# Performance work log

Hardware: AMD Instinct MI355X
Metric: run time of the kernel (lower is better)

## Reference

```python
import jax, jax.numpy as jnp
import numpy as np

NP, P, NS = 5, 5, 15  # body parts, joints per part, segments per scale


def _gauss_forward(x):
    # x: (batch, nb_frames, joints=NP*P, coordinates, 1)
    b, T, J, C, _ = x.shape
    inp = x.reshape(b, T, NP, P, C, 1)
    # lengths of the 6 temporal windows: full, two halves, three thirds
    seg_lens = [T, T // 2, T - T // 2, T // 3, T // 3, T - 2 * (T // 3)]
    outs = []
    for L in seg_lens:
        nb_fr = L // NS
        # first NS-1 segments of nb_fr frames each, always starting at frame 0
        head = inp[:, :(NS - 1) * nb_fr].reshape(b, NS - 1, nb_fr, NP, P, C, 1)
        mu_h = head.mean(axis=2)                    # (b, NS-1, NP, P, C, 1)
        xc = head - mu_h[:, :, None]
        cov_h = jnp.einsum('bkfnpci,bkfnpdi->bknpcd', xc, xc) / nb_fr
        # last segment runs to the END of the full sequence (faithful to original)
        tail = inp[:, (NS - 1) * nb_fr:]
        rest = tail.shape[1]
        mu_t = tail.mean(axis=1)                    # (b, NP, P, C, 1)
        xt = tail - mu_t[:, None]
        cov_t = jnp.einsum('bfnpci,bfnpdi->bnpcd', xt, xt) / rest
        mu = jnp.concatenate([mu_h, mu_t[:, None]], axis=1)    # (b, NS, NP, P, C, 1)
        cov = jnp.concatenate([cov_h, cov_t[:, None]], axis=1)  # (b, NS, NP, P, C, C)
        # match torch layout (b, NP, NS, P, ...)
        mu = jnp.transpose(mu, (0, 2, 1, 3, 4, 5))
        cov = jnp.transpose(cov, (0, 2, 1, 3, 4, 5))
        muT = jnp.swapaxes(mu, -1, -2)
        elt00 = cov + mu @ muT                       # E[xx^T]
        ones = jnp.ones(mu.shape[:-2] + (1, 1), dtype=x.dtype)
        top = jnp.concatenate([elt00, mu], axis=-1)
        bot = jnp.concatenate([muT, ones], axis=-1)
        outs.append(jnp.concatenate([top, bot], axis=-2))
    # (b, 6, NP, NS, P, C+1, C+1)
    return jnp.stack(outs, axis=1)


def setup_inputs() -> dict:
    key = jax.random.key(0)
    x = jax.random.normal(key, (256, 2048, 25, 3, 1), dtype=jnp.float32)
    return {"x": x}


def reference(x):
    return _gauss_forward(x)
```

## Files before the change

kernel.cpp:

```cpp
#include <hip/hip_runtime.h>
#include <hip/hip_bf16.h>
#include <stdint.h>


#define NPIECE_MAX 64
#define IDXPK 0x9210287517640543ull

struct Tab {
    int n;
    uint32_t p[NPIECE_MAX];
    uint32_t meta[NPIECE_MAX];
};

__global__ __launch_bounds__(1024) void fused_kernel(const float* __restrict__ x,
                                                     float* __restrict__ out, Tab tab) {
    __shared__ float sx[2][3760];
    __shared__ float red[6 * 225 + 16];
    int tid = threadIdx.x;
    int b   = blockIdx.x;
    const float* xb = x + (size_t)b * 153600;
    int wv = tid >> 6, ln = tid & 63;

    for (int i = tid; i < 6 * 225 + 16; i += 1024) red[i] = 0.f;

    {
        uint32_t pk = tab.p[0];
        int f0 = pk & 0xffff, L = (int)(pk >> 16);
        int w0 = f0 * 75, base_f = w0 & ~3;
        int nv4 = (w0 - base_f + L * 75 + 3) >> 2;
        const float4* src = (const float4*)(xb + base_f);
        int i = wv * 64 + ln;
        if (i < nv4)
            __builtin_amdgcn_global_load_lds(
                (const __attribute__((address_space(1))) void*)(src + i),
                (__attribute__((address_space(3))) void*)(&sx[0][wv * 256]), 16, 0, 0);
    }

    int cell = tid >> 2, q = tid & 3;
    int j  = cell / 9, si = cell - j * 9;
    int k3 = si - 3;
    int ia = (si < 3) ? si : (k3 < 3 ? 0 : (k3 < 5 ? 1 : 2));
    int ib = (si < 3) ? si : (k3 < 3 ? k3 : (k3 < 5 ? k3 - 2 : 2));
    bool single = (si < 3);
    int off0 = q * 75 + j * 3;

    __syncthreads();

    int n = tab.n;
    for (int p = 0; p < n; ++p) {
        uint32_t pk = tab.p[p];
        int f0 = pk & 0xffff, L = (int)(pk >> 16);
        int shift = (f0 * 75) & 3;
        int buf = p & 1;

        if (p + 1 < n) {
            uint32_t pk2 = tab.p[p + 1];
            int g0 = pk2 & 0xffff, L2 = (int)(pk2 >> 16);
            int w0 = g0 * 75, base_f = w0 & ~3;
            int nv4 = (w0 - base_f + L2 * 75 + 3) >> 2;
            const float4* src = (const float4*)(xb + base_f);
            int i = wv * 64 + ln;
            if (i < nv4)
                __builtin_amdgcn_global_load_lds(
                    (const __attribute__((address_space(1))) void*)(src + i),
                    (__attribute__((address_space(3))) void*)(&sx[buf ^ 1][wv * 256]), 16, 0, 0);
        }

        uint32_t mt = tab.meta[p];
        if (tid < 900) {
            const float* s = &sx[buf][shift];
            float acc = 0.f;
            int off = off0;
            for (int t = q; t < L; t += 4, off += 300) {
                float a  = s[off + ia];
                float bb = s[off + ib];
                acc += single ? a : a * bb;
            }
            acc += __shfl_xor(acc, 1);
            acc += __shfl_xor(acc, 2);
            if (q == 0) {
                int c0 = mt & 15, c1 = (mt >> 4) & 15, c2 = (mt >> 8) & 15;
                red[((c0 & 1)) * 225 + cell]     += acc;
                red[(2 + (c1 & 1)) * 225 + cell] += acc;
                red[(4 + (c2 & 1)) * 225 + cell] += acc;
            }
        }

        uint32_t em = (mt >> 12) & 7;
        if (em) {
            __syncthreads();
            float4* ob4 = (float4*)(out + (size_t)b * 36000);
            for (int st = 0; st < 3; ++st) {
                if (!((em >> st) & 1)) continue;
                int ch  = (mt >> (4 * st)) & 15;
                int ns  = (st == 0) ? 136 : (st == 1) ? 68 : 45;
                int nfr = (ch == 14) ? (2048 - 14 * ns) : ns;
                float inv = 1.0f / (float)nfr;
                int slot = st * 2 + (ch & 1);
                int ndup = st + 1;
                int so0  = (st == 0) ? 0 : (st == 1) ? 1 : 3;
                int tot  = ndup * 100;
                for (int i2 = tid; i2 < tot; i2 += 1024) {
                    int dup = i2 / 100;
                    int r2  = i2 - dup * 100;
                    int jj  = r2 >> 2, r = r2 & 3;
                    int np_ = jj / 5, pp = jj - np_ * 5;
                    const float* rb = &red[slot * 225 + jj * 9];
                    uint64_t pkk = IDXPK >> (16 * r);
                    float4 v;
                    v.x = rb[(int)(pkk & 15)] * inv;
                    v.y = rb[(int)((pkk >> 4) & 15)] * inv;
                    v.z = rb[(int)((pkk >> 8) & 15)] * inv;
                    v.w = (r == 3) ? 1.0f : rb[(int)((pkk >> 12) & 15)] * inv;
                    ob4[(so0 + dup) * 1500 + np_ * 300 + ch * 20 + pp * 4 + r] = v;
                }
            }
            __syncthreads();
            if (tid < 225) {
                for (int st = 0; st < 3; ++st) {
                    if (!((em >> st) & 1)) continue;
                    int ch = (mt >> (4 * st)) & 15;
                    red[(st * 2 + (ch & 1)) * 225 + tid] = 0.f;
                }
            }
        }
        __syncthreads();
    }
}

static void build_tab(Tab& tab) {
    unsigned char isb[2049];
    for (int i = 0; i <= 2048; ++i) isb[i] = 0;
    isb[2048] = 1;
    for (int k = 1; k <= 14; ++k) { isb[45 * k] = 1; isb[68 * k] = 1; isb[136 * k] = 1; }
    int n = 0, prev = 0;
    for (int f = 1; f <= 2048; ++f) {
        if (!isb[f]) continue;
        int len = f - prev;
        int npc = (len + 49) / 50;
        int base = len / npc, rem = len % npc;
        int s = prev;
        for (int i = 0; i < npc && n < NPIECE_MAX; ++i) {
            int l = base + (i < rem ? 1 : 0);
            tab.p[n++] = (uint32_t)(s | (l << 16));
            s += l;
        }
        prev = f;
    }
    tab.n = n;
    const int nst[3] = {136, 68, 45};
    for (int i = 0; i < n; ++i) {
        int f0 = tab.p[i] & 0xffff;
        int f1 = f0 + (int)(tab.p[i] >> 16);
        uint32_t m = 0;
        for (int st = 0; st < 3; ++st) {
            int ns = nst[st];
            int c = f0 / ns; if (c > 14) c = 14;
            int bnd = (c == 14) ? 2048 : (c + 1) * ns;
            m |= (uint32_t)c << (4 * st);
            if (f1 == bnd) m |= 1u << (12 + st);
        }
        tab.meta[i] = m;
    }
}

extern "C" void kernel_launch(void* const* d_in, const int* in_sizes, int n_in,
                              void* d_out, int out_size, void* d_ws, size_t ws_size,
                              hipStream_t stream) {
    const float* x = (const float*)d_in[0];
    float* out = (float*)d_out;
    Tab tab;
    build_tab(tab);
    fused_kernel<<<256, 1024, 0, stream>>>(x, out, tab);
}
```

Measured before the change: 251.0 us.

## Accumulate per-joint moments in registers with prefix marks, larger segments

Replaces the per-cell LDS accumulation (900 threads, 4 lanes per covariance entry) with 200 threads that each read a joint's three coordinates and accumulate all nine moments in registers. The running sums are differenced against per-scale marks at segment boundaries, so only the boundary pieces are reduced through shuffles. Pieces now span whole boundary-to-boundary intervals, with larger LDS buffers loaded in three chunks, which cuts the number of iterations and barriers. Output writes move to a single wave, and the barriers become raw s_waitcnt plus s_barrier. In exchange, only about 200 of 1024 threads do the compute, so per-thread serial work grows and parallelism drops.

```diff
diff --git a/kernel.cpp b/kernel.cpp
--- a/kernel.cpp
+++ b/kernel.cpp
@@ -1,111 +1,123 @@
 #include <hip/hip_runtime.h>
-#include <hip/hip_bf16.h>
 #include <stdint.h>
 
 
-#define NPIECE_MAX 64
+#define NSEG_MAX 40
 #define IDXPK 0x9210287517640543ull
 
 struct Tab {
     int n;
-    uint32_t p[NPIECE_MAX];
-    uint32_t meta[NPIECE_MAX];
+    uint32_t p[NSEG_MAX];
+    uint32_t meta[NSEG_MAX];
 };
 
-__global__ __launch_bounds__(1024) void fused_kernel(const float* __restrict__ x,
-                                                     float* __restrict__ out, Tab tab) {
-    __shared__ float sx[2][3760];
-    __shared__ float red[6 * 225 + 16];
+__device__ __forceinline__ void ebar() {
+    asm volatile("s_waitcnt lgkmcnt(0)\n\ts_barrier" ::: "memory");
+}
+
+__global__ __launch_bounds__(1024) void fused2(const float* __restrict__ x,
+                                               float* __restrict__ out, Tab tab) {
+    __shared__ float sx[2][10816];
+    __shared__ float red[240];
     int tid = threadIdx.x;
-    int b   = blockIdx.x;
+    int b = blockIdx.x;
     const float* xb = x + (size_t)b * 153600;
-    int wv = tid >> 6, ln = tid & 63;
+    int wv = tid >> 6;
 
-    for (int i = tid; i < 6 * 225 + 16; i += 1024) red[i] = 0.f;
+    float run[9], mark0[9], mark1[9], mark2[9];
+    #pragma unroll
+    for (int i = 0; i < 9; ++i) { run[i]=0.f; mark0[i]=0.f; mark1[i]=0.f; mark2[i]=0.f; }
+
+    int j = tid >> 3, ph = tid & 7;
 
     {
         uint32_t pk = tab.p[0];
         int f0 = pk & 0xffff, L = (int)(pk >> 16);
-        int w0 = f0 * 75, base_f = w0 & ~3;
-        int nv4 = (w0 - base_f + L * 75 + 3) >> 2;
-        const float4* src = (const float4*)(xb + base_f);
-        int i = wv * 64 + ln;
-        if (i < nv4)
-            __builtin_amdgcn_global_load_lds(
-                (const __attribute__((address_space(1))) void*)(src + i),
-                (__attribute__((address_space(3))) void*)(&sx[0][wv * 256]), 16, 0, 0);
+        int w0 = f0 * 75, bf = w0 & ~3;
+        int nv4 = (w0 - bf + L * 75 + 3) >> 2;
+        const float4* src = (const float4*)(xb + bf);
+        #pragma unroll
+        for (int k = 0; k < 3; ++k) {
+            int i = k * 1024 + tid;
+            if (i < nv4)
+                __builtin_amdgcn_global_load_lds(
+                    (const __attribute__((address_space(1))) void*)(src + i),
+                    (__attribute__((address_space(3))) void*)(&sx[0][(k * 1024 + wv * 64) * 4]),
+                    16, 0, 0);
+        }
     }
-
-    int cell = tid >> 2, q = tid & 3;
-    int j  = cell / 9, si = cell - j * 9;
-    int k3 = si - 3;
-    int ia = (si < 3) ? si : (k3 < 3 ? 0 : (k3 < 5 ? 1 : 2));
-    int ib = (si < 3) ? si : (k3 < 3 ? k3 : (k3 < 5 ? k3 - 2 : 2));
-    bool single = (si < 3);
-    int off0 = q * 75 + j * 3;
-
-    __syncthreads();
 
     int n = tab.n;
     for (int p = 0; p < n; ++p) {
+        __syncthreads();
+        int buf = p & 1;
+        if (p + 1 < n) {
+            uint32_t pk = tab.p[p + 1];
+            int f0 = pk & 0xffff, L = (int)(pk >> 16);
+            int w0 = f0 * 75, bf = w0 & ~3;
+            int nv4 = (w0 - bf + L * 75 + 3) >> 2;
+            const float4* src = (const float4*)(xb + bf);
+            #pragma unroll
+            for (int k = 0; k < 3; ++k) {
+                int i = k * 1024 + tid;
+                if (i < nv4)
+                    __builtin_amdgcn_global_load_lds(
+                        (const __attribute__((address_space(1))) void*)(src + i),
+                        (__attribute__((address_space(3))) void*)(&sx[buf ^ 1][(k * 1024 + wv * 64) * 4]),
+                        16, 0, 0);
+            }
+        }
+
         uint32_t pk = tab.p[p];
         int f0 = pk & 0xffff, L = (int)(pk >> 16);
-        int shift = (f0 * 75) & 3;
-        int buf = p & 1;
-
-        if (p + 1 < n) {
-            uint32_t pk2 = tab.p[p + 1];
-            int g0 = pk2 & 0xffff, L2 = (int)(pk2 >> 16);
-            int w0 = g0 * 75, base_f = w0 & ~3;
-            int nv4 = (w0 - base_f + L2 * 75 + 3) >> 2;
-            const float4* src = (const float4*)(xb + base_f);
-            int i = wv * 64 + ln;
-            if (i < nv4)
-                __builtin_amdgcn_global_load_lds(
-                    (const __attribute__((address_space(1))) void*)(src + i),
-                    (__attribute__((address_space(3))) void*)(&sx[buf ^ 1][wv * 256]), 16, 0, 0);
+        if (tid < 200) {
+            const float* s = &sx[buf][(f0 * 75) & 3];
+            int l0 = (ph - f0) & 7;
+            for (int l = l0; l < L; l += 8) {
+                const float* q = s + l * 75 + j * 3;
+                float a = q[0], bb = q[1], c = q[2];
+                run[0] += a;      run[1] += bb;     run[2] += c;
+                run[3] += a * a;  run[4] += a * bb; run[5] += a * c;
+                run[6] += bb * bb; run[7] += bb * c; run[8] += c * c;
+            }
         }
 
         uint32_t mt = tab.meta[p];
-        if (tid < 900) {
-            const float* s = &sx[buf][shift];
-            float acc = 0.f;
-            int off = off0;
-            for (int t = q; t < L; t += 4, off += 300) {
-                float a  = s[off + ia];
-                float bb = s[off + ib];
-                acc += single ? a : a * bb;
+        uint32_t em = mt >> 12;
+        for (int st = 0; st < 3; ++st) {
+            if (!((em >> st) & 1)) continue;
+            int ch = (mt >> (4 * st)) & 15;
+            if (tid < 200) {
+                float* mk = (st == 0) ? mark0 : (st == 1) ? mark1 : mark2;
+                float d[9];
+                #pragma unroll
+                for (int i = 0; i < 9; ++i) { d[i] = run[i] - mk[i]; mk[i] = run[i]; }
+                #pragma unroll
+                for (int i = 0; i < 9; ++i) {
+                    d[i] += __shfl_xor(d[i], 1);
+                    d[i] += __shfl_xor(d[i], 2);
+                    d[i] += __shfl_xor(d[i], 4);
+                }
+                float v = d[0];
+                #pragma unroll
+                for (int i = 1; i < 8; ++i) v = (ph == i) ? d[i] : v;
+                red[j * 9 + ph] = v;
+                if (ph == 0) red[j * 9 + 8] = d[8];
             }
-            acc += __shfl_xor(acc, 1);
-            acc += __shfl_xor(acc, 2);
-            if (q == 0) {
-                int c0 = mt & 15, c1 = (mt >> 4) & 15, c2 = (mt >> 8) & 15;
-                red[((c0 & 1)) * 225 + cell]     += acc;
-                red[(2 + (c1 & 1)) * 225 + cell] += acc;
-                red[(4 + (c2 & 1)) * 225 + cell] += acc;
-            }
-        }
-
-        uint32_t em = (mt >> 12) & 7;
-        if (em) {
-            __syncthreads();
-            float4* ob4 = (float4*)(out + (size_t)b * 36000);
-            for (int st = 0; st < 3; ++st) {
-                if (!((em >> st) & 1)) continue;
-                int ch  = (mt >> (4 * st)) & 15;
+            ebar();
+            if (wv == 15) {
                 int ns  = (st == 0) ? 136 : (st == 1) ? 68 : 45;
                 int nfr = (ch == 14) ? (2048 - 14 * ns) : ns;
                 float inv = 1.0f / (float)nfr;
-                int slot = st * 2 + (ch & 1);
-                int ndup = st + 1;
-                int so0  = (st == 0) ? 0 : (st == 1) ? 1 : 3;
-                int tot  = ndup * 100;
-                for (int i2 = tid; i2 < tot; i2 += 1024) {
-                    int dup = i2 / 100;
-                    int r2  = i2 - dup * 100;
-                    int jj  = r2 >> 2, r = r2 & 3;
+                int so0 = (st == 0) ? 0 : (st == 1) ? 1 : 3;
+                int Q = (st + 1) * 100;
+                float4* ob4 = (float4*)(out + (size_t)b * 36000);
+                int lane = tid - 960;
+                for (int q2 = lane; q2 < Q; q2 += 64) {
+                    int dup = q2 / 100, r2 = q2 - dup * 100;
+                    int jj = r2 >> 2, r = r2 & 3;
                     int np_ = jj / 5, pp = jj - np_ * 5;
-                    const float* rb = &red[slot * 225 + jj * 9];
+                    const float* rb = &red[jj * 9];
                     uint64_t pkk = IDXPK >> (16 * r);
                     float4 v;
                     v.x = rb[(int)(pkk & 15)] * inv;
@@ -115,16 +127,8 @@
                     ob4[(so0 + dup) * 1500 + np_ * 300 + ch * 20 + pp * 4 + r] = v;
                 }
             }
-            __syncthreads();
-            if (tid < 225) {
-                for (int st = 0; st < 3; ++st) {
-                    if (!((em >> st) & 1)) continue;
-                    int ch = (mt >> (4 * st)) & 15;
-                    red[(st * 2 + (ch & 1)) * 225 + tid] = 0.f;
-                }
-            }
+            ebar();
         }
-        __syncthreads();
     }
 }
 
@@ -133,35 +137,23 @@
     for (int i = 0; i <= 2048; ++i) isb[i] = 0;
     isb[2048] = 1;
     for (int k = 1; k <= 14; ++k) { isb[45 * k] = 1; isb[68 * k] = 1; isb[136 * k] = 1; }
+    const int nst[3] = {136, 68, 45};
     int n = 0, prev = 0;
     for (int f = 1; f <= 2048; ++f) {
         if (!isb[f]) continue;
-        int len = f - prev;
-        int npc = (len + 49) / 50;
-        int base = len / npc, rem = len % npc;
-        int s = prev;
-        for (int i = 0; i < npc && n < NPIECE_MAX; ++i) {
-            int l = base + (i < rem ? 1 : 0);
-            tab.p[n++] = (uint32_t)(s | (l << 16));
-            s += l;
+        tab.p[n] = (uint32_t)(prev | ((f - prev) << 16));
+        uint32_t m = 0;
+        for (int st = 0; st < 3; ++st) {
+            int ns = nst[st];
+            int c = prev / ns; if (c > 14) c = 14;
+            int bnd = (c == 14) ? 2048 : (c + 1) * ns;
+            m |= (uint32_t)c << (4 * st);
+            if (f == bnd) m |= 1u << (12 + st);
         }
+        tab.meta[n++] = m;
         prev = f;
     }
     tab.n = n;
-    const int nst[3] = {136, 68, 45};
-    for (int i = 0; i < n; ++i) {
-        int f0 = tab.p[i] & 0xffff;
-        int f1 = f0 + (int)(tab.p[i] >> 16);
-        uint32_t m = 0;
-        for (int st = 0; st < 3; ++st) {
-            int ns = nst[st];
-            int c = f0 / ns; if (c > 14) c = 14;
-            int bnd = (c == 14) ? 2048 : (c + 1) * ns;
-            m |= (uint32_t)c << (4 * st);
-            if (f1 == bnd) m |= 1u << (12 + st);
-        }
-        tab.meta[i] = m;
-    }
 }
 
 extern "C" void kernel_launch(void* const* d_in, const int* in_sizes, int n_in,
@@ -171,5 +163,5 @@
     float* out = (float*)d_out;
     Tab tab;
     build_tab(tab);
-    fused_kernel<<<256, 1024, 0, stream>>>(x, out, tab);
+    fused2<<<256, 1024, 0, stream>>>(x, out, tab);
 }
```

Measured after the change: 274.7 us. +9.4%, slower.
